# Performance work log

Hardware: AMD Instinct MI355X
Metric: run time of the kernel (lower is better)

## Reference

```python
import jax, jax.numpy as jnp
import numpy as np
import math

B, N, CS, CZ = 1, 512, 384, 128      # batch, residues, single-rep, pair-rep channels
H, C, NQP, NPV = 12, 16, 4, 8        # heads, head dim, query points, value points
W_C = math.sqrt(2.0 / (9.0 * NQP))
W_L = math.sqrt(1.0 / 3.0)

def _quat_to_rot(q):
    w, x, y, z = q[..., 0], q[..., 1], q[..., 2], q[..., 3]
    r0 = jnp.stack([1 - 2*(y*y + z*z), 2*(x*y - w*z), 2*(x*z + w*y)], -1)
    r1 = jnp.stack([2*(x*y + w*z), 1 - 2*(x*x + z*z), 2*(y*z - w*x)], -1)
    r2 = jnp.stack([2*(x*z - w*y), 2*(y*z + w*x), 1 - 2*(x*x + y*y)], -1)
    return jnp.stack([r0, r1, r2], -2)

def setup_inputs():
    key = jax.random.key(0)
    ks = jax.random.split(key, 16)
    s = jax.random.normal(ks[0], (B, N, CS), jnp.float32)
    z = jax.random.normal(ks[1], (B, N, N, CZ), jnp.float32)
    # rigid backbone transforms: rotation from unit quaternion + translation
    quat = jax.random.normal(ks[2], (B, N, 4), jnp.float32)
    quat = quat / jnp.linalg.norm(quat, axis=-1, keepdims=True)
    R = _quat_to_rot(quat)
    t = 10.0 * jax.random.normal(ks[3], (B, N, 3), jnp.float32)
    T = jnp.zeros((B, N, 4, 4), jnp.float32)
    T = T.at[..., :3, :3].set(R).at[..., :3, 3].set(t).at[..., 3, 3].set(1.0)
    def lin(k, fin, fout):
        k1, k2 = jax.random.split(k)
        return (0.02 * jax.random.normal(k1, (fin, fout), jnp.float32),
                0.02 * jax.random.normal(k2, (fout,), jnp.float32))
    Wq, bq = lin(ks[4], CS, H * C)
    Wk, bk = lin(ks[5], CS, H * C)
    Wv, bv = lin(ks[6], CS, H * C)
    Wqp, bqp = lin(ks[7], CS, 3 * H * NQP)
    Wkp, bkp = lin(ks[8], CS, 3 * H * NQP)
    Wvp, bvp = lin(ks[9], CS, 3 * H * NPV)
    Wb, bb = lin(ks[10], CZ, H)
    Wo, bo = lin(ks[11], H * (CZ + C + 4 * NPV), CS)
    head_weights = 0.1 * jax.random.normal(ks[12], (H,), jnp.float32)
    return dict(s=s, z=z, T=T, Wq=Wq, bq=bq, Wk=Wk, bk=bk, Wv=Wv, bv=bv,
                Wqp=Wqp, bqp=bqp, Wkp=Wkp, bkp=bkp, Wvp=Wvp, bvp=bvp,
                Wb=Wb, bb=bb, Wo=Wo, bo=bo, head_weights=head_weights)

def _forward(s, z, T, Wq, bq, Wk, bk, Wv, bv, Wqp, bqp, Wkp, bkp,
             Wvp, bvp, Wb, bb, Wo, bo, head_weights):
    R = T[..., :3, :3]                     # (B,N,3,3)
    t = T[..., :3, 3]                      # (B,N,3)
    # scalar q/k/v -> (B,H,N,C)
    q = jnp.transpose((s @ Wq + bq).reshape(B, N, H, C), (0, 2, 1, 3))
    k = jnp.transpose((s @ Wk + bk).reshape(B, N, H, C), (0, 2, 1, 3))
    v = jnp.transpose((s @ Wv + bv).reshape(B, N, H, C), (0, 2, 1, 3))
    # point q/k/v: (B,N,3,H,P) -> (B,H,P,N,3) (matches torch view+movedim order)
    def pts(Wp, bp, P):
        p = (s @ Wp + bp).reshape(B, N, 3, H, P)
        return jnp.transpose(p, (0, 3, 4, 1, 2))
    qp, kp, vp = pts(Wqp, bqp, NQP), pts(Wkp, bkp, NQP), pts(Wvp, bvp, NPV)
    # warp local points into global frame: x -> R_n x + t_n
    def warp(p):
        return jnp.einsum('bnxy,bhpny->bhpnx', R, p) + t[:, None, None]
    wq_pt, wk_pt, wv_pt = warp(qp), warp(kp), warp(vp)
    # attention logits
    qk = jnp.einsum('bhic,bhjc->bhij', q / math.sqrt(C), k)
    b_bias = jnp.transpose(z @ Wb + bb, (0, 3, 1, 2))          # (B,H,N,N)
    # sum_p ||wq_i - wk_j||^2 via norm expansion (avoids (B,H,P,3,N,N) tensor)
    qn = jnp.sum(wq_pt ** 2, axis=(-3, -1))                    # (B,H,N)
    kn = jnp.sum(wk_pt ** 2, axis=(-3, -1))
    qk_dot = jnp.einsum('bhpix,bhpjx->bhij', wq_pt, wk_pt)
    d2 = qn[..., :, None] + kn[..., None, :] - 2.0 * qk_dot
    gamma = jax.nn.softplus(head_weights)[:, None, None]       # (H,1,1)
    att = jax.nn.softmax(W_L * (qk + b_bias - gamma * W_C * d2 / 2.0), axis=-1)
    # outputs
    pairwise_out = jnp.einsum('bhij,bijc->bihc', att, z).reshape(B, N, H * CZ)
    v_out = jnp.einsum('bhij,bhjc->bihc', att, v).reshape(B, N, H * C)
    o_pt = jnp.einsum('bhij,bhpjx->bhpix', att, wv_pt)         # global-frame points
    # back to local frame of residue i: R_i^T (o - t_i)
    o_local = jnp.einsum('bnyx,bhpny->bhpnx', R, o_pt - t[:, None, None])
    o_local = jnp.einsum('bhpix->bixhp', o_local)              # (B,N,3,H,NPV)
    vp_out = o_local.reshape(B, N, 3 * H * NPV)
    vp_norm = jnp.linalg.norm(o_local, axis=-3).reshape(B, N, H * NPV)
    cat = jnp.concatenate([v_out, vp_out, vp_norm, pairwise_out], axis=-1)
    return cat @ Wo + bo

def reference(s, z, T, Wq, bq, Wk, bk, Wv, bv, Wqp, bqp, Wkp, bkp,
              Wvp, bvp, Wb, bb, Wo, bo, head_weights):
    return _forward(s, z, T, Wq, bq, Wk, bk, Wv, bv, Wqp, bqp, Wkp, bkp,
                    Wvp, bvp, Wb, bb, Wo, bo, head_weights)
```

## Files before the change

### kernel.cpp

```cpp
#include <hip/hip_runtime.h>
#include <hip/hip_bf16.h>
#include <math.h>

#define NRES 512
#define CS 384
#define CZ 128
#define NH 12
#define CC 16
#define NQP 4
#define NPV 8
#define HC (NH*CC)
#define FTOT 1152
#define CATF 2112
#define FSPLIT 8
#define FCHUNK 264
#define W_C 0.23570226039551584f
#define W_L 0.5773502691896258f

__global__ __launch_bounds__(384) void k_gemm(
    const float* __restrict__ s,
    const float* __restrict__ Wq, const float* __restrict__ bq,
    const float* __restrict__ Wk, const float* __restrict__ bk,
    const float* __restrict__ Wv, const float* __restrict__ bv,
    const float* __restrict__ Wqp, const float* __restrict__ bqp,
    const float* __restrict__ Wkp, const float* __restrict__ bkp,
    const float* __restrict__ Wvp, const float* __restrict__ bvp,
    float* __restrict__ p_raw)
{
    int r0 = blockIdx.x * 8;
    int f  = blockIdx.y * 384 + threadIdx.x;
    const float* W; const float* bia; int col; int stride;
    if      (f < 192) { W = Wq;  bia = bq;  col = f;       stride = 192; }
    else if (f < 384) { W = Wk;  bia = bk;  col = f - 192; stride = 192; }
    else if (f < 576) { W = Wv;  bia = bv;  col = f - 384; stride = 192; }
    else if (f < 720) { W = Wqp; bia = bqp; col = f - 576; stride = 144; }
    else if (f < 864) { W = Wkp; bia = bkp; col = f - 720; stride = 144; }
    else              { W = Wvp; bia = bvp; col = f - 864; stride = 288; }

    float acc[8];
    float b0 = bia[col];
    #pragma unroll
    for (int j = 0; j < 8; ++j) acc[j] = b0;

    const float* srow = s + (size_t)r0 * CS;
    #pragma unroll 4
    for (int i = 0; i < CS; ++i) {
        float w = W[(size_t)i * stride + col];
        #pragma unroll
        for (int j = 0; j < 8; ++j) acc[j] = fmaf(w, srow[j*CS + i], acc[j]);
    }
    #pragma unroll
    for (int j = 0; j < 8; ++j) p_raw[(size_t)(r0 + j)*FTOT + f] = acc[j];
}

__global__ __launch_bounds__(256) void k_post(
    const float* __restrict__ p_raw, const float* __restrict__ T,
    float* __restrict__ q_s, float4* __restrict__ k_t4, float4* __restrict__ v_t4,
    float* __restrict__ wq, float4* __restrict__ wk_t4, float4* __restrict__ wv_t4,
    float* __restrict__ qn, float* __restrict__ kn)
{
    int n = blockIdx.x;
    int tid = threadIdx.x;
    __shared__ float pl[FTOT];
    __shared__ float Rl[9], tl[3];
    __shared__ float wq_l[144], wk_l[144], wv_l[288];
    __shared__ float sq_part[48], sk_part[48];

    for (int idx = tid; idx < FTOT/4; idx += 256)
        *reinterpret_cast<float4*>(&pl[idx*4]) =
            *reinterpret_cast<const float4*>(&p_raw[(size_t)n*FTOT + idx*4]);
    if (tid < 9)  Rl[tid] = T[n*16 + (tid/3)*4 + (tid%3)];
    if (tid >= 16 && tid < 19) tl[tid-16] = T[n*16 + (tid-16)*4 + 3];
    __syncthreads();

    if (tid < 48) {
        int h = tid >> 2, p = tid & 3;
        float qy0 = pl[576 + 0*48 + h*4 + p], qy1 = pl[576 + 1*48 + h*4 + p], qy2 = pl[576 + 2*48 + h*4 + p];
        float ky0 = pl[720 + 0*48 + h*4 + p], ky1 = pl[720 + 1*48 + h*4 + p], ky2 = pl[720 + 2*48 + h*4 + p];
        float qs2 = 0.f, ks2 = 0.f;
        #pragma unroll
        for (int x = 0; x < 3; ++x) {
            float wqv = Rl[x*3+0]*qy0 + Rl[x*3+1]*qy1 + Rl[x*3+2]*qy2 + tl[x];
            float wkv = Rl[x*3+0]*ky0 + Rl[x*3+1]*ky1 + Rl[x*3+2]*ky2 + tl[x];
            wq_l[h*12 + p*3 + x] = wqv;
            wk_l[h*12 + p*3 + x] = wkv;
            qs2 += wqv*wqv; ks2 += wkv*wkv;
        }
        sq_part[tid] = qs2; sk_part[tid] = ks2;
    } else if (tid >= 64 && tid < 160) {
        int u = tid - 64; int h = u >> 3, p = u & 7;
        float y0 = pl[864 + 0*96 + h*8 + p], y1 = pl[864 + 1*96 + h*8 + p], y2 = pl[864 + 2*96 + h*8 + p];
        #pragma unroll
        for (int x = 0; x < 3; ++x) {
            wv_l[h*24 + p*3 + x] = Rl[x*3+0]*y0 + Rl[x*3+1]*y1 + Rl[x*3+2]*y2 + tl[x];
        }
    }
    __syncthreads();

    if (tid < 48) {
        int h = tid >> 2, c4 = tid & 3;
        float4 qv = *reinterpret_cast<const float4*>(&pl[h*16 + c4*4]);
        qv.x *= 0.25f; qv.y *= 0.25f; qv.z *= 0.25f; qv.w *= 0.25f;
        float4 kv = *reinterpret_cast<const float4*>(&pl[192 + h*16 + c4*4]);
        float4 vv = *reinterpret_cast<const float4*>(&pl[384 + h*16 + c4*4]);
        *reinterpret_cast<float4*>(&q_s[((size_t)h*NRES + n)*16 + c4*4]) = qv;
        k_t4[((size_t)h*4 + c4)*NRES + n] = kv;
        v_t4[((size_t)h*4 + c4)*NRES + n] = vv;
    } else if (tid >= 64 && tid < 100) {
        int u = tid - 64; int h = u / 3, e4 = u % 3;
        float4 kv = *reinterpret_cast<const float4*>(&wk_l[h*12 + e4*4]);
        wk_t4[((size_t)h*3 + e4)*NRES + n] = kv;
    } else if (tid >= 104 && tid < 140) {
        int u = tid - 104; int h = u / 3, e4 = u % 3;
        float4 qv = *reinterpret_cast<const float4*>(&wq_l[h*12 + e4*4]);
        *reinterpret_cast<float4*>(&wq[((size_t)h*NRES + n)*12 + e4*4]) = qv;
    } else if (tid >= 160 && tid < 232) {
        int u = tid - 160; int h = u / 6, e4 = u % 6;
        float4 vv = *reinterpret_cast<const float4*>(&wv_l[h*24 + e4*4]);
        wv_t4[((size_t)h*6 + e4)*NRES + n] = vv;
    } else if (tid >= 232 && tid < 244) {
        int h = tid - 232;
        qn[(size_t)h*NRES + n] = sq_part[h*4] + sq_part[h*4+1] + sq_part[h*4+2] + sq_part[h*4+3];
        kn[(size_t)h*NRES + n] = sk_part[h*4] + sk_part[h*4+1] + sk_part[h*4+2] + sk_part[h*4+3];
    }
}

__global__ __launch_bounds__(256) void k_bias(
    const float* __restrict__ z, const float* __restrict__ Wb,
    const float* __restrict__ bb, float* __restrict__ bias)
{
    int j0 = blockIdx.x * 64, i = blockIdx.y;
    int tid = threadIdx.x;
    int r = tid & 63, p = tid >> 6;
    __shared__ float zl[64*132];
    __shared__ float wbl[12*128];
    __shared__ float partial[4][12][64];
    __shared__ float bbl[12];

    for (int idx = tid; idx < 1536; idx += 256) {
        int h = idx >> 7, c = idx & 127;
        wbl[idx] = Wb[c*12 + h];
    }
    if (tid < 12) bbl[tid] = bb[tid];
    const float4* zsrc = reinterpret_cast<const float4*>(z + ((size_t)i*NRES + j0)*CZ);
    #pragma unroll
    for (int it = 0; it < 8; ++it) {
        int idx = it*256 + tid;
        int j = idx >> 5, c4 = idx & 31;
        *reinterpret_cast<float4*>(&zl[j*132 + c4*4]) = zsrc[idx];
    }
    __syncthreads();

    float acc[12] = {0,0,0,0,0,0,0,0,0,0,0,0};
    #pragma unroll 2
    for (int it = 0; it < 8; ++it) {
        int c4 = p*8 + it;
        float4 zv = *reinterpret_cast<const float4*>(&zl[r*132 + c4*4]);
        #pragma unroll
        for (int h = 0; h < 12; ++h) {
            float4 wv = *reinterpret_cast<const float4*>(&wbl[h*128 + c4*4]);
            acc[h] = fmaf(zv.x, wv.x, fmaf(zv.y, wv.y, fmaf(zv.z, wv.z, fmaf(zv.w, wv.w, acc[h]))));
        }
    }
    #pragma unroll
    for (int h = 0; h < 12; ++h) partial[p][h][r] = acc[h];
    __syncthreads();

    #pragma unroll
    for (int u = 0; u < 3; ++u) {
        int idx = u*256 + tid;
        int h = idx >> 6, rr = idx & 63;
        float v = partial[0][h][rr] + partial[1][h][rr]
                + partial[2][h][rr] + partial[3][h][rr] + bbl[h];
        bias[((size_t)h*NRES + i)*NRES + j0 + rr] = v;
    }
}

__global__ __launch_bounds__(256) void k_att(
    const float* __restrict__ q_s, const float4* __restrict__ k_t4,
    const float* __restrict__ wq, const float4* __restrict__ wk_t4,
    const float* __restrict__ qn, const float* __restrict__ kn,
    const float* __restrict__ hw, const float* __restrict__ T,
    float* __restrict__ bias,
    const float4* __restrict__ v_t4, const float4* __restrict__ wv_t4,
    float* __restrict__ cat)
{
    int i = blockIdx.x, h = blockIdx.y;
    int tid = threadIdx.x;
    __shared__ float ql[16], wql[12];
    __shared__ float att[NRES];
    __shared__ float red[8];
    __shared__ float optl[24];
    __shared__ float sG, sQn;

    if (tid < 16) ql[tid] = q_s[((size_t)h*NRES + i)*16 + tid];
    else if (tid < 28) wql[tid-16] = wq[((size_t)h*NRES + i)*12 + (tid-16)];
    if (tid == 0) {
        sQn = qn[(size_t)h*NRES + i];
        float x = hw[h];
        float sp = (x > 20.f) ? x : log1pf(expf(x));
        sG = sp * W_C * 0.5f;
    }
    __syncthreads();
    float qn_i = sQn, gam = sG;

    float lg[2];
    #pragma unroll
    for (int m = 0; m < 2; ++m) {
        int j = tid + m*256;
        float qk = 0.f;
        #pragma unroll
        for (int c4 = 0; c4 < 4; ++c4) {
            float4 kv = k_t4[((size_t)h*4 + c4)*NRES + j];
            qk += ql[c4*4+0]*kv.x + ql[c4*4+1]*kv.y + ql[c4*4+2]*kv.z + ql[c4*4+3]*kv.w;
        }
        float dd = 0.f;
        #pragma unroll
        for (int e4 = 0; e4 < 3; ++e4) {
            float4 kv = wk_t4[((size_t)h*3 + e4)*NRES + j];
            dd += wql[e4*4+0]*kv.x + wql[e4*4+1]*kv.y + wql[e4*4+2]*kv.z + wql[e4*4+3]*kv.w;
        }
        float d2 = qn_i + kn[(size_t)h*NRES + j] - 2.f*dd;
        lg[m] = W_L * (qk + bias[((size_t)h*NRES + i)*NRES + j] - gam*d2);
    }

    int wave = tid >> 6, lane = tid & 63;
    float mx = fmaxf(lg[0], lg[1]);
    #pragma unroll
    for (int d = 32; d > 0; d >>= 1) mx = fmaxf(mx, __shfl_xor(mx, d));
    if (lane == 0) red[wave] = mx;
    __syncthreads();
    mx = fmaxf(fmaxf(red[0], red[1]), fmaxf(red[2], red[3]));
    float e0 = __expf(lg[0]-mx), e1 = __expf(lg[1]-mx);
    float sm = e0 + e1;
    #pragma unroll
    for (int d = 32; d > 0; d >>= 1) sm += __shfl_xor(sm, d);
    if (lane == 0) red[4+wave] = sm;
    __syncthreads();
    float inv = 1.f / (red[4]+red[5]+red[6]+red[7]);
    float a0 = e0*inv, a1 = e1*inv;
    att[tid] = a0; att[tid+256] = a1;
    bias[((size_t)h*NRES + i)*NRES + tid]       = a0;
    bias[((size_t)h*NRES + i)*NRES + tid + 256] = a1;
    __syncthreads();

    for (int g = wave; g < 10; g += 4) {
        const float4* row = (g < 4) ? &v_t4[((size_t)h*4 + g)*NRES]
                                    : &wv_t4[((size_t)h*6 + (g-4))*NRES];
        float px = 0.f, py = 0.f, pz = 0.f, pw = 0.f;
        #pragma unroll
        for (int jj = 0; jj < 8; ++jj) {
            int j = lane + jj*64;
            float a = att[j];
            float4 r = row[j];
            px += a*r.x; py += a*r.y; pz += a*r.z; pw += a*r.w;
        }
        #pragma unroll
        for (int d = 32; d > 0; d >>= 1) {
            px += __shfl_down(px, d);
            py += __shfl_down(py, d);
            pz += __shfl_down(pz, d);
            pw += __shfl_down(pw, d);
        }
        if (lane == 0) {
            if (g < 4) {
                *reinterpret_cast<float4*>(&cat[(size_t)i*CATF + h*16 + g*4]) =
                    make_float4(px, py, pz, pw);
            } else {
                int e = (g-4)*4;
                optl[e] = px; optl[e+1] = py; optl[e+2] = pz; optl[e+3] = pw;
            }
        }
    }
    __syncthreads();

    if (tid < 8) {
        int p = tid;
        float t0 = T[i*16 + 0*4 + 3], t1 = T[i*16 + 1*4 + 3], t2 = T[i*16 + 2*4 + 3];
        float y0 = optl[p*3+0] - t0, y1 = optl[p*3+1] - t1, y2 = optl[p*3+2] - t2;
        float n2 = 0.f;
        #pragma unroll
        for (int x = 0; x < 3; ++x) {
            float w = T[i*16 + 0*4 + x]*y0 + T[i*16 + 1*4 + x]*y1 + T[i*16 + 2*4 + x]*y2;
            cat[(size_t)i*CATF + 192 + x*96 + h*8 + p] = w;
            n2 += w*w;
        }
        cat[(size_t)i*CATF + 480 + h*8 + p] = sqrtf(n2);
    }
}

__global__ __launch_bounds__(256) void k_pair(
    const float* __restrict__ z, const float* __restrict__ att,
    float* __restrict__ cat)
{
    int i = blockIdx.x, tid = threadIdx.x;
    __shared__ float zl[64*129];
    __shared__ float al[12*64];
    int c = tid & 127, hh = tid >> 7;
    float acc[6] = {0,0,0,0,0,0};
    for (int j0 = 0; j0 < NRES; j0 += 64) {
        __syncthreads();
        for (int idx = tid; idx < 64*128; idx += 256) {
            int j = idx >> 7, cc = idx & 127;
            zl[j*129 + cc] = z[((size_t)i*NRES + j0 + j)*CZ + cc];
        }
        for (int idx = tid; idx < 12*64; idx += 256) {
            int h2 = idx >> 6, jj = idx & 63;
            al[h2*64 + jj] = att[((size_t)h2*NRES + i)*NRES + j0 + jj];
        }
        __syncthreads();
        for (int jj = 0; jj < 64; ++jj) {
            float zv = zl[jj*129 + c];
            #pragma unroll
            for (int m = 0; m < 6; ++m) {
                acc[m] += al[(hh + 2*m)*64 + jj] * zv;
            }
        }
    }
    #pragma unroll
    for (int m = 0; m < 6; ++m) {
        cat[(size_t)i*CATF + 576 + (hh + 2*m)*128 + c] = acc[m];
    }
}

__global__ __launch_bounds__(384) void k_wo(
    const float* __restrict__ cat, const float* __restrict__ Wo,
    float* __restrict__ part)
{
    int i0 = blockIdx.x * 8;
    int fs = blockIdx.y;
    int f0 = fs * FCHUNK;
    int tid = threadIdx.x;
    __shared__ float cl[8][FCHUNK];
    for (int idx = tid; idx < 8*(FCHUNK/4); idx += 384) {
        int j = idx / (FCHUNK/4), q = idx % (FCHUNK/4);
        *reinterpret_cast<float4*>(&cl[j][q*4]) =
            *reinterpret_cast<const float4*>(&cat[(size_t)(i0+j)*CATF + f0 + q*4]);
    }
    __syncthreads();
    float acc[8] = {0,0,0,0,0,0,0,0};
    const float* wp = Wo + (size_t)f0*CS + tid;
    #pragma unroll 4
    for (int f = 0; f < FCHUNK; ++f) {
        float w = wp[(size_t)f*CS];
        #pragma unroll
        for (int j = 0; j < 8; ++j) acc[j] = fmaf(w, cl[j][f], acc[j]);
    }
    #pragma unroll
    for (int j = 0; j < 8; ++j)
        part[((size_t)fs*NRES + i0 + j)*CS + tid] = acc[j];
}

__global__ __launch_bounds__(384) void k_red(
    const float* __restrict__ part, const float* __restrict__ bo,
    float* __restrict__ out)
{
    int i = blockIdx.x, o = threadIdx.x;
    float a = bo[o];
    #pragma unroll
    for (int s = 0; s < FSPLIT; ++s)
        a += part[((size_t)s*NRES + i)*CS + o];
    out[(size_t)i*CS + o] = a;
}

extern "C" void kernel_launch(void* const* d_in, const int* in_sizes, int n_in,
                              void* d_out, int out_size, void* d_ws, size_t ws_size,
                              hipStream_t stream)
{
    const float* s   = (const float*)d_in[0];
    const float* z   = (const float*)d_in[1];
    const float* T   = (const float*)d_in[2];
    const float* Wq  = (const float*)d_in[3];  const float* bq  = (const float*)d_in[4];
    const float* Wk  = (const float*)d_in[5];  const float* bk  = (const float*)d_in[6];
    const float* Wv  = (const float*)d_in[7];  const float* bv  = (const float*)d_in[8];
    const float* Wqp = (const float*)d_in[9];  const float* bqp = (const float*)d_in[10];
    const float* Wkp = (const float*)d_in[11]; const float* bkp = (const float*)d_in[12];
    const float* Wvp = (const float*)d_in[13]; const float* bvp = (const float*)d_in[14];
    const float* Wb  = (const float*)d_in[15]; const float* bb  = (const float*)d_in[16];
    const float* Wo  = (const float*)d_in[17]; const float* bo  = (const float*)d_in[18];
    const float* hw  = (const float*)d_in[19];
    float* out = (float*)d_out;
    float* ws  = (float*)d_ws;

    size_t off = 0;
    float* q_s  = ws + off; off += (size_t)NH*NRES*CC;
    float* k_t  = ws + off; off += (size_t)NH*NRES*CC;
    float* v_t  = ws + off; off += (size_t)NH*NRES*CC;
    float* wq   = ws + off; off += (size_t)NH*NRES*12;
    float* wk_t = ws + off; off += (size_t)NH*NRES*12;
    float* wv_t = ws + off; off += (size_t)NH*NRES*24;
    float* qn   = ws + off; off += (size_t)NH*NRES;
    float* kn   = ws + off; off += (size_t)NH*NRES;
    float* bias = ws + off; off += (size_t)NH*NRES*NRES;
    float* cat  = ws + off; off += (size_t)NRES*CATF;
    float* part = ws + off; off += (size_t)FSPLIT*NRES*CS;
    float* praw = ws + off; off += (size_t)NRES*FTOT;

    k_gemm<<<dim3(NRES/8, 3), dim3(384), 0, stream>>>(
        s, Wq, bq, Wk, bk, Wv, bv, Wqp, bqp, Wkp, bkp, Wvp, bvp, praw);

    k_post<<<dim3(NRES), dim3(256), 0, stream>>>(
        praw, T, q_s, (float4*)k_t, (float4*)v_t, wq, (float4*)wk_t, (float4*)wv_t, qn, kn);

    k_bias<<<dim3(8, NRES), dim3(256), 0, stream>>>(z, Wb, bb, bias);

    k_att<<<dim3(NRES, NH), dim3(256), 0, stream>>>(
        q_s, (const float4*)k_t, wq, (const float4*)wk_t, qn, kn, hw, T, bias,
        (const float4*)v_t, (const float4*)wv_t, cat);

    k_pair<<<dim3(NRES), dim3(256), 0, stream>>>(z, bias, cat);

    k_wo<<<dim3(NRES/8, FSPLIT), dim3(384), 0, stream>>>(cat, Wo, part);

    k_red<<<dim3(NRES), dim3(384), 0, stream>>>(part, bo, out);
}
```

Before: 186.4 us.

## Process two query rows per attention block and restructure pair aggregation

The attention kernel now handles two query residues per block, so each loaded key, point and value vector is reused for both rows and the grid halves. The pairwise-output kernel drops the shared-memory staging of z and streams z directly as float4 from global memory. Each of four thread groups covers a quarter of the residues, and the partial sums are reduced through shared memory afterwards. This removes the z tile copies and the barriers between them, at the cost of more registers in the attention kernel and a larger shared attention buffer in the pair kernel.

```diff
diff --git a/kernel.cpp b/kernel.cpp
--- a/kernel.cpp
+++ b/kernel.cpp
@@ -185,99 +185,126 @@
     const float4* __restrict__ v_t4, const float4* __restrict__ wv_t4,
     float* __restrict__ cat)
 {
-    int i = blockIdx.x, h = blockIdx.y;
+    int i0 = blockIdx.x * 2, h = blockIdx.y;
     int tid = threadIdx.x;
-    __shared__ float ql[16], wql[12];
-    __shared__ float att[NRES];
-    __shared__ float red[8];
-    __shared__ float optl[24];
-    __shared__ float sG, sQn;
-
-    if (tid < 16) ql[tid] = q_s[((size_t)h*NRES + i)*16 + tid];
-    else if (tid < 28) wql[tid-16] = wq[((size_t)h*NRES + i)*12 + (tid-16)];
-    if (tid == 0) {
-        sQn = qn[(size_t)h*NRES + i];
+    int wave = tid >> 6, lane = tid & 63;
+    __shared__ float ql[2][16], wql[2][12];
+    __shared__ float att[2][NRES];
+    __shared__ float redm[2][4], reds[2][4];
+    __shared__ float optl[2][24];
+    __shared__ float sQn[2], sG;
+
+    if (tid < 32) {
+        int ii = tid >> 4, c = tid & 15;
+        ql[ii][c] = q_s[((size_t)h*NRES + i0+ii)*16 + c];
+    } else if (tid < 56) {
+        int u = tid - 32; int ii = u / 12, e = u % 12;
+        wql[ii][e] = wq[((size_t)h*NRES + i0+ii)*12 + e];
+    } else if (tid < 58) {
+        int ii = tid - 56;
+        sQn[ii] = qn[(size_t)h*NRES + i0+ii];
+    } else if (tid == 58) {
         float x = hw[h];
         float sp = (x > 20.f) ? x : log1pf(expf(x));
         sG = sp * W_C * 0.5f;
     }
     __syncthreads();
-    float qn_i = sQn, gam = sG;
-
-    float lg[2];
+    float gam = sG;
+
+    float lg[2][2];
     #pragma unroll
     for (int m = 0; m < 2; ++m) {
         int j = tid + m*256;
-        float qk = 0.f;
-        #pragma unroll
-        for (int c4 = 0; c4 < 4; ++c4) {
-            float4 kv = k_t4[((size_t)h*4 + c4)*NRES + j];
-            qk += ql[c4*4+0]*kv.x + ql[c4*4+1]*kv.y + ql[c4*4+2]*kv.z + ql[c4*4+3]*kv.w;
-        }
-        float dd = 0.f;
-        #pragma unroll
-        for (int e4 = 0; e4 < 3; ++e4) {
-            float4 kv = wk_t4[((size_t)h*3 + e4)*NRES + j];
-            dd += wql[e4*4+0]*kv.x + wql[e4*4+1]*kv.y + wql[e4*4+2]*kv.z + wql[e4*4+3]*kv.w;
-        }
-        float d2 = qn_i + kn[(size_t)h*NRES + j] - 2.f*dd;
-        lg[m] = W_L * (qk + bias[((size_t)h*NRES + i)*NRES + j] - gam*d2);
-    }
-
-    int wave = tid >> 6, lane = tid & 63;
-    float mx = fmaxf(lg[0], lg[1]);
-    #pragma unroll
-    for (int d = 32; d > 0; d >>= 1) mx = fmaxf(mx, __shfl_xor(mx, d));
-    if (lane == 0) red[wave] = mx;
-    __syncthreads();
-    mx = fmaxf(fmaxf(red[0], red[1]), fmaxf(red[2], red[3]));
-    float e0 = __expf(lg[0]-mx), e1 = __expf(lg[1]-mx);
-    float sm = e0 + e1;
-    #pragma unroll
-    for (int d = 32; d > 0; d >>= 1) sm += __shfl_xor(sm, d);
-    if (lane == 0) red[4+wave] = sm;
-    __syncthreads();
-    float inv = 1.f / (red[4]+red[5]+red[6]+red[7]);
-    float a0 = e0*inv, a1 = e1*inv;
-    att[tid] = a0; att[tid+256] = a1;
-    bias[((size_t)h*NRES + i)*NRES + tid]       = a0;
-    bias[((size_t)h*NRES + i)*NRES + tid + 256] = a1;
+        float4 kv0 = k_t4[((size_t)h*4 + 0)*NRES + j];
+        float4 kv1 = k_t4[((size_t)h*4 + 1)*NRES + j];
+        float4 kv2 = k_t4[((size_t)h*4 + 2)*NRES + j];
+        float4 kv3 = k_t4[((size_t)h*4 + 3)*NRES + j];
+        float4 wv0 = wk_t4[((size_t)h*3 + 0)*NRES + j];
+        float4 wv1 = wk_t4[((size_t)h*3 + 1)*NRES + j];
+        float4 wv2 = wk_t4[((size_t)h*3 + 2)*NRES + j];
+        float knj = kn[(size_t)h*NRES + j];
+        #pragma unroll
+        for (int ii = 0; ii < 2; ++ii) {
+            float qk = ql[ii][0]*kv0.x + ql[ii][1]*kv0.y + ql[ii][2]*kv0.z + ql[ii][3]*kv0.w
+                     + ql[ii][4]*kv1.x + ql[ii][5]*kv1.y + ql[ii][6]*kv1.z + ql[ii][7]*kv1.w
+                     + ql[ii][8]*kv2.x + ql[ii][9]*kv2.y + ql[ii][10]*kv2.z + ql[ii][11]*kv2.w
+                     + ql[ii][12]*kv3.x + ql[ii][13]*kv3.y + ql[ii][14]*kv3.z + ql[ii][15]*kv3.w;
+            float dd = wql[ii][0]*wv0.x + wql[ii][1]*wv0.y + wql[ii][2]*wv0.z + wql[ii][3]*wv0.w
+                     + wql[ii][4]*wv1.x + wql[ii][5]*wv1.y + wql[ii][6]*wv1.z + wql[ii][7]*wv1.w
+                     + wql[ii][8]*wv2.x + wql[ii][9]*wv2.y + wql[ii][10]*wv2.z + wql[ii][11]*wv2.w;
+            float d2 = sQn[ii] + knj - 2.f*dd;
+            lg[ii][m] = W_L * (qk + bias[((size_t)h*NRES + i0+ii)*NRES + j] - gam*d2);
+        }
+    }
+
+    #pragma unroll
+    for (int ii = 0; ii < 2; ++ii) {
+        float mx = fmaxf(lg[ii][0], lg[ii][1]);
+        #pragma unroll
+        for (int d = 32; d > 0; d >>= 1) mx = fmaxf(mx, __shfl_xor(mx, d));
+        if (lane == 0) redm[ii][wave] = mx;
+    }
+    __syncthreads();
+    #pragma unroll
+    for (int ii = 0; ii < 2; ++ii) {
+        float mx = fmaxf(fmaxf(redm[ii][0], redm[ii][1]), fmaxf(redm[ii][2], redm[ii][3]));
+        float e0 = __expf(lg[ii][0]-mx), e1 = __expf(lg[ii][1]-mx);
+        lg[ii][0] = e0; lg[ii][1] = e1;
+        float sm = e0 + e1;
+        #pragma unroll
+        for (int d = 32; d > 0; d >>= 1) sm += __shfl_xor(sm, d);
+        if (lane == 0) reds[ii][wave] = sm;
+    }
+    __syncthreads();
+    #pragma unroll
+    for (int ii = 0; ii < 2; ++ii) {
+        float inv = 1.f / (reds[ii][0]+reds[ii][1]+reds[ii][2]+reds[ii][3]);
+        float a0 = lg[ii][0]*inv, a1 = lg[ii][1]*inv;
+        att[ii][tid] = a0; att[ii][tid+256] = a1;
+        bias[((size_t)h*NRES + i0+ii)*NRES + tid]       = a0;
+        bias[((size_t)h*NRES + i0+ii)*NRES + tid + 256] = a1;
+    }
     __syncthreads();
 
     for (int g = wave; g < 10; g += 4) {
         const float4* row = (g < 4) ? &v_t4[((size_t)h*4 + g)*NRES]
                                     : &wv_t4[((size_t)h*6 + (g-4))*NRES];
-        float px = 0.f, py = 0.f, pz = 0.f, pw = 0.f;
-        #pragma unroll
-        for (int jj = 0; jj < 8; ++jj) {
-            int j = lane + jj*64;
-            float a = att[j];
-            float4 r = row[j];
-            px += a*r.x; py += a*r.y; pz += a*r.z; pw += a*r.w;
+        float p0x=0,p0y=0,p0z=0,p0w=0, p1x=0,p1y=0,p1z=0,p1w=0;
+        #pragma unroll
+        for (int u = 0; u < 8; ++u) {
+            int jr = lane + u*64;
+            float4 r = row[jr];
+            float a0 = att[0][jr], a1 = att[1][jr];
+            p0x += a0*r.x; p0y += a0*r.y; p0z += a0*r.z; p0w += a0*r.w;
+            p1x += a1*r.x; p1y += a1*r.y; p1z += a1*r.z; p1w += a1*r.w;
         }
         #pragma unroll
         for (int d = 32; d > 0; d >>= 1) {
-            px += __shfl_down(px, d);
-            py += __shfl_down(py, d);
-            pz += __shfl_down(pz, d);
-            pw += __shfl_down(pw, d);
+            p0x += __shfl_down(p0x, d); p0y += __shfl_down(p0y, d);
+            p0z += __shfl_down(p0z, d); p0w += __shfl_down(p0w, d);
+            p1x += __shfl_down(p1x, d); p1y += __shfl_down(p1y, d);
+            p1z += __shfl_down(p1z, d); p1w += __shfl_down(p1w, d);
         }
         if (lane == 0) {
             if (g < 4) {
-                *reinterpret_cast<float4*>(&cat[(size_t)i*CATF + h*16 + g*4]) =
-                    make_float4(px, py, pz, pw);
+                *reinterpret_cast<float4*>(&cat[(size_t)(i0+0)*CATF + h*16 + g*4]) =
+                    make_float4(p0x, p0y, p0z, p0w);
+                *reinterpret_cast<float4*>(&cat[(size_t)(i0+1)*CATF + h*16 + g*4]) =
+                    make_float4(p1x, p1y, p1z, p1w);
             } else {
                 int e = (g-4)*4;
-                optl[e] = px; optl[e+1] = py; optl[e+2] = pz; optl[e+3] = pw;
+                optl[0][e] = p0x; optl[0][e+1] = p0y; optl[0][e+2] = p0z; optl[0][e+3] = p0w;
+                optl[1][e] = p1x; optl[1][e+1] = p1y; optl[1][e+2] = p1z; optl[1][e+3] = p1w;
             }
         }
     }
     __syncthreads();
 
-    if (tid < 8) {
-        int p = tid;
+    if (tid < 16) {
+        int ii = tid >> 3, p = tid & 7;
+        int i = i0 + ii;
         float t0 = T[i*16 + 0*4 + 3], t1 = T[i*16 + 1*4 + 3], t2 = T[i*16 + 2*4 + 3];
-        float y0 = optl[p*3+0] - t0, y1 = optl[p*3+1] - t1, y2 = optl[p*3+2] - t2;
+        float y0 = optl[ii][p*3+0] - t0, y1 = optl[ii][p*3+1] - t1, y2 = optl[ii][p*3+2] - t2;
         float n2 = 0.f;
         #pragma unroll
         for (int x = 0; x < 3; ++x) {
@@ -289,37 +316,55 @@
     }
 }
 
-__global__ __launch_bounds__(256) void k_pair(
+__global__ __launch_bounds__(512) void k_pair(
     const float* __restrict__ z, const float* __restrict__ att,
     float* __restrict__ cat)
 {
     int i = blockIdx.x, tid = threadIdx.x;
-    __shared__ float zl[64*129];
-    __shared__ float al[12*64];
-    int c = tid & 127, hh = tid >> 7;
-    float acc[6] = {0,0,0,0,0,0};
-    for (int j0 = 0; j0 < NRES; j0 += 64) {
-        __syncthreads();
-        for (int idx = tid; idx < 64*128; idx += 256) {
-            int j = idx >> 7, cc = idx & 127;
-            zl[j*129 + cc] = z[((size_t)i*NRES + j0 + j)*CZ + cc];
-        }
-        for (int idx = tid; idx < 12*64; idx += 256) {
-            int h2 = idx >> 6, jj = idx & 63;
-            al[h2*64 + jj] = att[((size_t)h2*NRES + i)*NRES + j0 + jj];
-        }
-        __syncthreads();
-        for (int jj = 0; jj < 64; ++jj) {
-            float zv = zl[jj*129 + c];
-            #pragma unroll
-            for (int m = 0; m < 6; ++m) {
-                acc[m] += al[(hh + 2*m)*64 + jj] * zv;
-            }
-        }
-    }
-    #pragma unroll
-    for (int m = 0; m < 6; ++m) {
-        cat[(size_t)i*CATF + 576 + (hh + 2*m)*128 + c] = acc[m];
+    int us = tid >> 7, ht = (tid >> 5) & 3, c4 = tid & 31;
+    __shared__ float al[12*NRES];
+
+    for (int idx = tid; idx < 12*NRES; idx += 512) {
+        int h = idx >> 9, j = idx & 511;
+        al[idx] = att[((size_t)h*NRES + i)*NRES + j];
+    }
+    __syncthreads();
+
+    const float4* z4 = reinterpret_cast<const float4*>(z + (size_t)i*NRES*CZ);
+    float4 a0 = {0,0,0,0}, a1 = {0,0,0,0}, a2 = {0,0,0,0};
+    int ub = us*128;
+    #pragma unroll 4
+    for (int u = 0; u < 128; ++u) {
+        int jr = ub + u;
+        float4 zv = z4[(size_t)jr*32 + c4];
+        float w0 = al[(ht    )*NRES + jr];
+        float w1 = al[(ht + 4)*NRES + jr];
+        float w2 = al[(ht + 8)*NRES + jr];
+        a0.x = fmaf(w0, zv.x, a0.x); a0.y = fmaf(w0, zv.y, a0.y);
+        a0.z = fmaf(w0, zv.z, a0.z); a0.w = fmaf(w0, zv.w, a0.w);
+        a1.x = fmaf(w1, zv.x, a1.x); a1.y = fmaf(w1, zv.y, a1.y);
+        a1.z = fmaf(w1, zv.z, a1.z); a1.w = fmaf(w1, zv.w, a1.w);
+        a2.x = fmaf(w2, zv.x, a2.x); a2.y = fmaf(w2, zv.y, a2.y);
+        a2.z = fmaf(w2, zv.z, a2.z); a2.w = fmaf(w2, zv.w, a2.w);
+    }
+    __syncthreads();
+    float* pr = al;
+    {
+        float* p = &pr[tid*12];
+        p[0]=a0.x; p[1]=a0.y; p[2]=a0.z;  p[3]=a0.w;
+        p[4]=a1.x; p[5]=a1.y; p[6]=a1.z;  p[7]=a1.w;
+        p[8]=a2.x; p[9]=a2.y; p[10]=a2.z; p[11]=a2.w;
+    }
+    __syncthreads();
+
+    for (int idx = tid; idx < 1536; idx += 512) {
+        int h = idx >> 7, c = idx & 127;
+        int hh = h & 3, m = h >> 2, cc4 = c >> 2, x = c & 3;
+        float v = 0.f;
+        #pragma unroll
+        for (int uu = 0; uu < 4; ++uu)
+            v += pr[(((uu*4 + hh)*32 + cc4))*12 + m*4 + x];
+        cat[(size_t)i*CATF + 576 + h*128 + c] = v;
     }
 }
 
@@ -404,11 +449,11 @@
 
     k_bias<<<dim3(8, NRES), dim3(256), 0, stream>>>(z, Wb, bb, bias);
 
-    k_att<<<dim3(NRES, NH), dim3(256), 0, stream>>>(
+    k_att<<<dim3(NRES/2, NH), dim3(256), 0, stream>>>(
         q_s, (const float4*)k_t, wq, (const float4*)wk_t, qn, kn, hw, T, bias,
         (const float4*)v_t, (const float4*)wv_t, cat);
 
-    k_pair<<<dim3(NRES), dim3(256), 0, stream>>>(z, bias, cat);
+    k_pair<<<dim3(NRES), dim3(512), 0, stream>>>(z, bias, cat);
 
     k_wo<<<dim3(NRES/8, FSPLIT), dim3(384), 0, stream>>>(cat, Wo, part);
 
```

Measured after the change: 165.8 us. 11.1% less time.
